# Optimization experiments

Measured on AMD Instinct MI355X. Metric: run time of the kernel, lower is better.

Reference implementation:

```python
import jax, jax.numpy as jnp
import numpy as np

B, T, E, H = 4, 2048, 1024, 16
HD = E // H  # head_size = 64


def setup_inputs() -> dict:
    key = jax.random.key(0)
    ks = jax.random.split(key, 6)
    s = 1.0 / np.sqrt(E)
    x = jax.random.normal(ks[0], (B, T, E), dtype=jnp.float32)
    # per-head Q/K/V projection weights, stacked over heads: [H, E, HD]
    Wq = jax.random.uniform(ks[1], (H, E, HD), minval=-s, maxval=s, dtype=jnp.float32)
    Wk = jax.random.uniform(ks[2], (H, E, HD), minval=-s, maxval=s, dtype=jnp.float32)
    Wv = jax.random.uniform(ks[3], (H, E, HD), minval=-s, maxval=s, dtype=jnp.float32)
    Wo = jax.random.uniform(ks[4], (E, E), minval=-s, maxval=s, dtype=jnp.float32)
    bo = jax.random.uniform(ks[5], (E,), minval=-s, maxval=s, dtype=jnp.float32)
    return {"x": x, "Wq": Wq, "Wk": Wk, "Wv": Wv, "Wo": Wo, "bo": bo}


def reference(x, Wq, Wk, Wv, Wo, bo):
    # x: [B,T,E] -> q,k,v: [B,H,T,HD]
    q = jnp.einsum('bte,hed->bhtd', x, Wq)
    k = jnp.einsum('bte,hed->bhtd', x, Wk)
    v = jnp.einsum('bte,hed->bhtd', x, Wv)
    scale = HD ** -0.5
    scores = jnp.einsum('bhtd,bhsd->bhts', q, k) * scale  # [B,H,T,T]
    causal = jnp.tril(jnp.ones((T, T), dtype=bool))
    scores = jnp.where(causal, scores, -jnp.inf)
    wei = jax.nn.softmax(scores, axis=-1)  # dropout is identity in eval
    out = jnp.einsum('bhts,bhsd->bhtd', wei, v)  # [B,H,T,HD]
    out = out.transpose(0, 2, 1, 3).reshape(B, T, E)  # concat heads
    return out @ Wo.T + bo
```

## Files before the change

kernel.cpp:

```cpp
#include <hip/hip_runtime.h>
#include <hip/hip_bf16.h>

#define B_  4
#define T_  2048
#define E_  1024
#define H_  16
#define HD_ 64

typedef __hip_bfloat16 bf16;
typedef unsigned short u16;
using bf16x8 = __attribute__((ext_vector_type(8))) short;
using f32x4  = __attribute__((ext_vector_type(4))) float;

__device__ __forceinline__ float b2f(bf16 x) { return __bfloat162float(x); }
__device__ __forceinline__ bf16  f2b(float x) { return __float2bfloat16(x); }
__device__ __forceinline__ u16 f2b_bits(float x) {
    union { bf16 h; u16 u; } cv; cv.h = __float2bfloat16(x); return cv.u;
}
__device__ __forceinline__ float bits2f(u16 u) {
    union { float f; unsigned int i; } cv; cv.i = ((unsigned int)u) << 16; return cv.f;
}

__device__ __forceinline__ void gld_lds16(const void* g, void* lds) {
    void* gv = (void*)g;
    __builtin_amdgcn_global_load_lds(
        (__attribute__((address_space(1))) void*)gv,
        (__attribute__((address_space(3))) void*)lds, 16, 0, 0);
}

__global__ __launch_bounds__(256) void cast_bf16(
    const float* __restrict__ src, bf16* __restrict__ dst)
{
    size_t i = ((size_t)blockIdx.x * 256 + threadIdx.x) * 8;
    float4 a = *(const float4*)(src + i);
    float4 b = *(const float4*)(src + i + 4);
    u16 o[8] = { f2b_bits(a.x), f2b_bits(a.y), f2b_bits(a.z), f2b_bits(a.w),
                 f2b_bits(b.x), f2b_bits(b.y), f2b_bits(b.z), f2b_bits(b.w) };
    *(uint4*)(dst + i) = *(const uint4*)o;
}

__global__ __launch_bounds__(256) void cast_w_t(
    const float* __restrict__ Wq, const float* __restrict__ Wk,
    const float* __restrict__ Wv, bf16* __restrict__ Wt)
{
    const float* W = (blockIdx.z == 0) ? Wq : (blockIdx.z == 1) ? Wk : Wv;
    const float scl = (blockIdx.z == 0) ? 0.125f : 1.0f;
    bf16* dst = Wt + (size_t)blockIdx.z * (H_ * HD_ * E_);
    const int h = blockIdx.y, k0 = blockIdx.x * 64;
    __shared__ float Ws[64][65];
    const int tid = threadIdx.x;
    {
        int kk = tid >> 2, d0 = (tid & 3) * 16;
        const float* p = W + ((size_t)h * E_ + k0 + kk) * HD_ + d0;
        #pragma unroll
        for (int i = 0; i < 4; i++) {
            float4 f = *(const float4*)(p + i * 4);
            Ws[kk][d0 + i * 4 + 0] = f.x; Ws[kk][d0 + i * 4 + 1] = f.y;
            Ws[kk][d0 + i * 4 + 2] = f.z; Ws[kk][d0 + i * 4 + 3] = f.w;
        }
    }
    __syncthreads();
    {
        int d = tid >> 2, kc = (tid & 3) * 16;
        u16 o[16];
        #pragma unroll
        for (int j = 0; j < 16; j++) o[j] = f2b_bits(Ws[kc + j][d] * scl);
        bf16* p = dst + ((size_t)h * HD_ + d) * E_ + k0 + kc;
        *(uint4*)(p)     = *(const uint4*)&o[0];
        *(uint4*)(p + 8) = *(const uint4*)&o[8];
    }
}

__global__ __launch_bounds__(256) void qkv_mfma(
    const bf16* __restrict__ xb, const bf16* __restrict__ Wt,
    bf16* __restrict__ q, bf16* __restrict__ k, bf16* __restrict__ v)
{
    const int n0 = blockIdx.x * 128;
    const int m0 = blockIdx.y * 128;
    const int z  = n0 >> 10;
    bf16* out = (z == 0) ? q : (z == 1) ? k : v;
    const int tid = threadIdx.x, lane = tid & 63, w = tid >> 6;
    const int wm = w >> 1, wn = w & 1;
    const int quad = lane >> 4, l15 = lane & 15;

    __shared__ __align__(16) u16 smem[2 * 128 * 64];
    u16* As = smem;
    u16* Bs = smem + 128 * 64;

    f32x4 acc[4][4];
    #pragma unroll
    for (int i = 0; i < 4; i++)
        #pragma unroll
        for (int j = 0; j < 4; j++) acc[i][j] = f32x4{0.f, 0.f, 0.f, 0.f};

    const int srow = lane >> 3;
    const int scol = ((lane & 7) ^ srow) * 8;
    const bf16* agp = xb + (size_t)(m0 + w * 32 + srow) * E_ + scol;
    const bf16* bgp = Wt + (size_t)(n0 + w * 32 + srow) * E_ + scol;
    u16* alds = As + (w * 32) * 64;
    u16* blds = Bs + (w * 32) * 64;
    const int rsw = l15 & 7;

    for (int k0 = 0; k0 < E_; k0 += 64) {
        __syncthreads();
        #pragma unroll
        for (int i = 0; i < 4; i++) {
            gld_lds16(agp + (size_t)(i * 8) * E_ + k0, alds + i * 8 * 64);
            gld_lds16(bgp + (size_t)(i * 8) * E_ + k0, blds + i * 8 * 64);
        }
        __syncthreads();

        #pragma unroll
        for (int ks = 0; ks < 2; ks++) {
            const int csw = ((ks * 4 + quad) ^ rsw) * 8;
            bf16x8 af[4];
            #pragma unroll
            for (int i = 0; i < 4; i++)
                af[i] = *(const bf16x8*)&As[(wm * 64 + i * 16 + l15) * 64 + csw];
            #pragma unroll
            for (int j = 0; j < 4; j++) {
                bf16x8 bfr = *(const bf16x8*)&Bs[(wn * 64 + j * 16 + l15) * 64 + csw];
                #pragma unroll
                for (int i = 0; i < 4; i++)
                    acc[i][j] = __builtin_amdgcn_mfma_f32_16x16x32_bf16(af[i], bfr, acc[i][j], 0, 0, 0);
            }
        }
    }

    if (z != 2) {
        const int h = ((n0 & 1023) >> 6) + wn;
        #pragma unroll
        for (int i = 0; i < 4; i++)
            #pragma unroll
            for (int r = 0; r < 4; r++) {
                int m = m0 + wm * 64 + i * 16 + quad * 4 + r;
                int bb2 = m >> 11, t = m & (T_ - 1);
                bf16* orow = out + ((size_t)(bb2 * H_ + h) * T_ + t) * HD_;
                #pragma unroll
                for (int j = 0; j < 4; j++)
                    orow[j * 16 + l15] = f2b(acc[i][j][r]);
            }
    } else {
        u16 (*Vt)[136] = (u16(*)[136])smem;
        const int bb2 = m0 >> 11, t0 = m0 & (T_ - 1);
        #pragma unroll
        for (int half = 0; half < 2; half++) {
            __syncthreads();
            if (wn == half) {
                #pragma unroll
                for (int j = 0; j < 4; j++)
                    #pragma unroll
                    for (int i = 0; i < 4; i++) {
                        ushort4 pk;
                        pk.x = f2b_bits(acc[i][j][0]);
                        pk.y = f2b_bits(acc[i][j][1]);
                        pk.z = f2b_bits(acc[i][j][2]);
                        pk.w = f2b_bits(acc[i][j][3]);
                        *(ushort4*)&Vt[j * 16 + l15][wm * 64 + i * 16 + quad * 4] = pk;
                    }
            }
            __syncthreads();
            {
                int dd = tid >> 2, tt = (tid & 3) * 32;
                int h = ((n0 & 1023) >> 6) + half;
                bf16* dst = out + ((size_t)(bb2 * H_ + h) * HD_ + dd) * T_ + t0 + tt;
                #pragma unroll
                for (int u = 0; u < 4; u++)
                    *(uint4*)(dst + u * 8) = *(const uint4*)&Vt[dd][tt + u * 8];
            }
        }
    }
}

__global__ __launch_bounds__(256) void flash_attn(
    const bf16* __restrict__ q, const bf16* __restrict__ k,
    const bf16* __restrict__ vt, bf16* __restrict__ att)
{
    const int bh = blockIdx.x & 63;
    const int qt = 31 - (blockIdx.x >> 6);
    const int q0 = qt * 64;
    const int hh = bh & 15, bb = bh >> 4;
    const int tid = threadIdx.x, lane = tid & 63, wave = tid >> 6;
    const int quad = lane >> 4, l15 = lane & 15;

    __shared__ __align__(16) u16 Ks[64 * 64];
    __shared__ __align__(16) u16 Vs[64 * 64];
    __shared__ __align__(16) u16 P2[4 * 1024];

    const size_t baseK = (size_t)bh * T_ * HD_;
    const bf16* vbase = vt + (size_t)bh * (size_t)HD_ * T_;

    const int qg = q0 + wave * 16 + l15;
    const bf16* qrow = q + baseK + (size_t)qg * HD_;
    bf16x8 qfrag[2];
    qfrag[0] = *(const bf16x8*)(qrow + quad * 8);
    qfrag[1] = *(const bf16x8*)(qrow + 32 + quad * 8);

    f32x4 o[4];
    #pragma unroll
    for (int dt = 0; dt < 4; dt++) o[dt] = f32x4{0.f, 0.f, 0.f, 0.f};
    float l_i = 0.f;

    const int q_in = wave * 16 + l15;

    const int srow = lane >> 3;
    const int scol = ((lane & 7) ^ srow) * 8;
    const bf16* kgp = k + baseK + (size_t)(wave * 16 + srow) * HD_ + scol;
    const bf16* vgp = vbase + (size_t)(wave * 16 + srow) * T_ + scol;
    u16* klds = Ks + wave * 16 * 64;
    u16* vlds = Vs + wave * 16 * 64;
    u16* pw = P2 + wave * 1024;
    const int rsw = l15 & 7;

    for (int st = 0; st <= qt; st++) {
        const int s0 = st * 64;
        __syncthreads();
        #pragma unroll
        for (int i = 0; i < 2; i++) {
            gld_lds16(kgp + (size_t)(s0 + i * 8) * HD_, klds + i * 8 * 64);
            gld_lds16(vgp + (size_t)(i * 8) * T_ + s0, vlds + i * 8 * 64);
        }
        __syncthreads();

        f32x4 s[4];
        #pragma unroll
        for (int ct = 0; ct < 4; ct++) {
            f32x4 a = f32x4{0.f, 0.f, 0.f, 0.f};
            #pragma unroll
            for (int ks = 0; ks < 2; ks++) {
                const int csw = ((ks * 4 + quad) ^ rsw) * 8;
                bf16x8 kfrag = *(const bf16x8*)&Ks[(ct * 16 + l15) * 64 + csw];
                a = __builtin_amdgcn_mfma_f32_16x16x32_bf16(kfrag, qfrag[ks], a, 0, 0, 0);
            }
            s[ct] = a;
        }

        if (st == qt) {
            #pragma unroll
            for (int ct = 0; ct < 4; ct++) {
                int sbase = ct * 16 + quad * 4;
                #pragma unroll
                for (int r = 0; r < 4; r++)
                    if (sbase + r > q_in) s[ct][r] = -1e30f;
            }
        }

        float rsum = 0.f;
        #pragma unroll
        for (int ct = 0; ct < 4; ct++) {
            ushort4 pk;
            pk.x = f2b_bits(__expf(s[ct][0] - 8.0f));
            pk.y = f2b_bits(__expf(s[ct][1] - 8.0f));
            pk.z = f2b_bits(__expf(s[ct][2] - 8.0f));
            pk.w = f2b_bits(__expf(s[ct][3] - 8.0f));
            rsum += bits2f(pk.x) + bits2f(pk.y) + bits2f(pk.z) + bits2f(pk.w);
            *(ushort4*)&pw[(ct >> 1) * 512
                           + (((((ct & 1) << 1) | (quad >> 1)) * 16 + l15) * 8)
                           + (quad & 1) * 4] = pk;
        }
        rsum += __shfl_xor(rsum, 16, 64);
        rsum += __shfl_xor(rsum, 32, 64);
        l_i += rsum;

        #pragma unroll
        for (int ks = 0; ks < 2; ks++) {
            bf16x8 pfrag = *(const bf16x8*)&pw[ks * 512 + (quad * 16 + l15) * 8];
            #pragma unroll
            for (int dt = 0; dt < 4; dt++) {
                const int csw = ((ks * 4 + quad) ^ rsw) * 8;
                bf16x8 vfrag = *(const bf16x8*)&Vs[(dt * 16 + l15) * 64 + csw];
                o[dt] = __builtin_amdgcn_mfma_f32_16x16x32_bf16(vfrag, pfrag, o[dt], 0, 0, 0);
            }
        }
    }

    float inv = 1.0f / l_i;
    bf16* orow = att + ((size_t)(bb * T_ + qg) * H_ + hh) * HD_;
    #pragma unroll
    for (int dt = 0; dt < 4; dt++) {
        ushort4 pk;
        pk.x = f2b_bits(o[dt][0] * inv);
        pk.y = f2b_bits(o[dt][1] * inv);
        pk.z = f2b_bits(o[dt][2] * inv);
        pk.w = f2b_bits(o[dt][3] * inv);
        *(ushort4*)(orow + dt * 16 + quad * 4) = pk;
    }
}

__global__ __launch_bounds__(256, 3) void out_proj_mfma(
    const bf16* __restrict__ att, const bf16* __restrict__ Wob,
    const float* __restrict__ bo, float* __restrict__ out)
{
    const int m0 = blockIdx.x * 128, n0 = blockIdx.y * 128;
    const int tid = threadIdx.x, lane = tid & 63, w = tid >> 6;
    const int wm = w >> 1, wn = w & 1;
    const int quad = lane >> 4, l15 = lane & 15;

    __shared__ __align__(16) u16 As[128 * 32];
    __shared__ __align__(16) u16 Bs[128 * 32];

    f32x4 acc[4][4];
    #pragma unroll
    for (int i = 0; i < 4; i++)
        #pragma unroll
        for (int j = 0; j < 4; j++) acc[i][j] = f32x4{0.f, 0.f, 0.f, 0.f};

    const int srow = lane >> 2;
    const int scol = ((lane & 3) ^ (srow & 3)) * 8;
    const bf16* agp = att + (size_t)(m0 + w * 32 + srow) * E_ + scol;
    const bf16* bgp = Wob + (size_t)(n0 + w * 32 + srow) * E_ + scol;
    u16* alds = As + (w * 32) * 32;
    u16* blds = Bs + (w * 32) * 32;
    const int rsw3 = l15 & 3;

    for (int k0 = 0; k0 < E_; k0 += 32) {
        __syncthreads();
        #pragma unroll
        for (int i = 0; i < 2; i++) {
            gld_lds16(agp + (size_t)(i * 16) * E_ + k0, alds + i * 16 * 32);
            gld_lds16(bgp + (size_t)(i * 16) * E_ + k0, blds + i * 16 * 32);
        }
        __syncthreads();

        const int csw = (quad ^ rsw3) * 8;
        bf16x8 af[4];
        #pragma unroll
        for (int i = 0; i < 4; i++)
            af[i] = *(const bf16x8*)&As[(wm * 64 + i * 16 + l15) * 32 + csw];
        #pragma unroll
        for (int j = 0; j < 4; j++) {
            bf16x8 bfr = *(const bf16x8*)&Bs[(wn * 64 + j * 16 + l15) * 32 + csw];
            #pragma unroll
            for (int i = 0; i < 4; i++)
                acc[i][j] = __builtin_amdgcn_mfma_f32_16x16x32_bf16(af[i], bfr, acc[i][j], 0, 0, 0);
        }
    }

    float bias[4];
    #pragma unroll
    for (int j = 0; j < 4; j++) bias[j] = bo[n0 + wn * 64 + j * 16 + l15];
    #pragma unroll
    for (int i = 0; i < 4; i++)
        #pragma unroll
        for (int r = 0; r < 4; r++) {
            int m = m0 + wm * 64 + i * 16 + quad * 4 + r;
            float* orow = out + (size_t)m * E_ + n0 + wn * 64;
            #pragma unroll
            for (int j = 0; j < 4; j++)
                orow[j * 16 + l15] = acc[i][j][r] + bias[j];
        }
}

extern "C" void kernel_launch(void* const* d_in, const int* in_sizes, int n_in,
                              void* d_out, int out_size, void* d_ws, size_t ws_size,
                              hipStream_t stream)
{
    const float* x  = (const float*)d_in[0];
    const float* Wq = (const float*)d_in[1];
    const float* Wk = (const float*)d_in[2];
    const float* Wv = (const float*)d_in[3];
    const float* Wo = (const float*)d_in[4];
    const float* bo = (const float*)d_in[5];
    float* out = (float*)d_out;

    const size_t elts = (size_t)B_ * H_ * T_ * HD_;
    bf16* att = (bf16*)d_ws;
    bf16* Wt  = att;
    bf16* q   = att + elts;
    bf16* Wob = q;
    bf16* k   = q + elts;
    bf16* v   = k + elts;
    bf16* xb  = (bf16*)d_out;

    cast_bf16<<<dim3((unsigned)(elts / 2048)), 256, 0, stream>>>(x, xb);
    cast_w_t<<<dim3(E_ / 64, H_, 3), 256, 0, stream>>>(Wq, Wk, Wv, Wt);

    qkv_mfma<<<dim3(3 * E_ / 128, (B_ * T_) / 128), 256, 0, stream>>>(xb, Wt, q, k, v);

    flash_attn<<<dim3((T_ / 64) * B_ * H_), 256, 0, stream>>>(q, k, v, att);

    cast_bf16<<<dim3((E_ * E_) / 2048), 256, 0, stream>>>(Wo, Wob);

    out_proj_mfma<<<dim3((B_ * T_) / 128, E_ / 128), 256, 0, stream>>>(att, Wob, bo, out);
}
```

Before: 253.2 us.

## Double-buffer K/V tiles in flash attention and compute row sums via MFMA

Adds double-buffered LDS for the K and V tiles so that the global-to-LDS load of the next tile is issued before computing on the current one, using an explicit vmcnt wait and raw barriers in place of two __syncthreads per step. The softmax row sum is now produced by an extra MFMA against a vector of ones instead of per-lane adds and cross-lane shuffles. The exponential is rewritten as exp2 of a fused multiply-add, and setprio hints are placed around the MFMA sections. LDS use grows to hold the second buffer, which could lower occupancy, and correctness relies on the hand-written waitcnt count matching the number of issued loads.

```diff
diff --git a/kernel.cpp b/kernel.cpp
--- a/kernel.cpp
+++ b/kernel.cpp
@@ -183,9 +183,9 @@
     const int tid = threadIdx.x, lane = tid & 63, wave = tid >> 6;
     const int quad = lane >> 4, l15 = lane & 15;
 
-    __shared__ __align__(16) u16 Ks[64 * 64];
-    __shared__ __align__(16) u16 Vs[64 * 64];
-    __shared__ __align__(16) u16 P2[4 * 1024];
+    __shared__ __align__(16) u16 Ks[2][64 * 64];
+    __shared__ __align__(16) u16 Vs[2][64 * 64];
+    __shared__ __align__(16) u16 P2[4][1024];
 
     const size_t baseK = (size_t)bh * T_ * HD_;
     const bf16* vbase = vt + (size_t)bh * (size_t)HD_ * T_;
@@ -196,10 +196,14 @@
     qfrag[0] = *(const bf16x8*)(qrow + quad * 8);
     qfrag[1] = *(const bf16x8*)(qrow + 32 + quad * 8);
 
+    bf16x8 onesf;
+    #pragma unroll
+    for (int i = 0; i < 8; i++) onesf[i] = (short)0x3F80;
+
     f32x4 o[4];
     #pragma unroll
     for (int dt = 0; dt < 4; dt++) o[dt] = f32x4{0.f, 0.f, 0.f, 0.f};
-    float l_i = 0.f;
+    f32x4 lacc = f32x4{0.f, 0.f, 0.f, 0.f};
 
     const int q_in = wave * 16 + l15;
 
@@ -207,33 +211,43 @@
     const int scol = ((lane & 7) ^ srow) * 8;
     const bf16* kgp = k + baseK + (size_t)(wave * 16 + srow) * HD_ + scol;
     const bf16* vgp = vbase + (size_t)(wave * 16 + srow) * T_ + scol;
-    u16* klds = Ks + wave * 16 * 64;
-    u16* vlds = Vs + wave * 16 * 64;
-    u16* pw = P2 + wave * 1024;
+    u16* pw = P2[wave];
     const int rsw = l15 & 7;
 
+    #define STAGE(b, s0) do {                                                 \
+        gld_lds16(kgp + (size_t)(s0) * HD_,       &Ks[b][wave * 1024]);       \
+        gld_lds16(kgp + (size_t)((s0) + 8) * HD_, &Ks[b][wave * 1024 + 512]); \
+        gld_lds16(vgp + (s0),                     &Vs[b][wave * 1024]);       \
+        gld_lds16(vgp + (s0) + 8 * T_,            &Vs[b][wave * 1024 + 512]); \
+    } while (0)
+
+    STAGE(0, 0);
+    int cur = 0;
+
     for (int st = 0; st <= qt; st++) {
-        const int s0 = st * 64;
-        __syncthreads();
-        #pragma unroll
-        for (int i = 0; i < 2; i++) {
-            gld_lds16(kgp + (size_t)(s0 + i * 8) * HD_, klds + i * 8 * 64);
-            gld_lds16(vgp + (size_t)(i * 8) * T_ + s0, vlds + i * 8 * 64);
-        }
-        __syncthreads();
+        if (st < qt) {
+            STAGE(cur ^ 1, (st + 1) * 64);
+            asm volatile("s_waitcnt vmcnt(4)" ::: "memory");
+        } else {
+            asm volatile("s_waitcnt vmcnt(0)" ::: "memory");
+        }
+        __builtin_amdgcn_s_barrier();
+        __builtin_amdgcn_sched_barrier(0);
 
         f32x4 s[4];
+        __builtin_amdgcn_s_setprio(1);
         #pragma unroll
         for (int ct = 0; ct < 4; ct++) {
             f32x4 a = f32x4{0.f, 0.f, 0.f, 0.f};
             #pragma unroll
             for (int ks = 0; ks < 2; ks++) {
                 const int csw = ((ks * 4 + quad) ^ rsw) * 8;
-                bf16x8 kfrag = *(const bf16x8*)&Ks[(ct * 16 + l15) * 64 + csw];
+                bf16x8 kfrag = *(const bf16x8*)&Ks[cur][(ct * 16 + l15) * 64 + csw];
                 a = __builtin_amdgcn_mfma_f32_16x16x32_bf16(kfrag, qfrag[ks], a, 0, 0, 0);
             }
             s[ct] = a;
         }
+        __builtin_amdgcn_s_setprio(0);
 
         if (st == qt) {
             #pragma unroll
@@ -245,36 +259,39 @@
             }
         }
 
-        float rsum = 0.f;
         #pragma unroll
         for (int ct = 0; ct < 4; ct++) {
             ushort4 pk;
-            pk.x = f2b_bits(__expf(s[ct][0] - 8.0f));
-            pk.y = f2b_bits(__expf(s[ct][1] - 8.0f));
-            pk.z = f2b_bits(__expf(s[ct][2] - 8.0f));
-            pk.w = f2b_bits(__expf(s[ct][3] - 8.0f));
-            rsum += bits2f(pk.x) + bits2f(pk.y) + bits2f(pk.z) + bits2f(pk.w);
+            pk.x = f2b_bits(__builtin_amdgcn_exp2f(__fmaf_rn(s[ct][0], 1.4426950408889634f, -11.541560327111707f)));
+            pk.y = f2b_bits(__builtin_amdgcn_exp2f(__fmaf_rn(s[ct][1], 1.4426950408889634f, -11.541560327111707f)));
+            pk.z = f2b_bits(__builtin_amdgcn_exp2f(__fmaf_rn(s[ct][2], 1.4426950408889634f, -11.541560327111707f)));
+            pk.w = f2b_bits(__builtin_amdgcn_exp2f(__fmaf_rn(s[ct][3], 1.4426950408889634f, -11.541560327111707f)));
             *(ushort4*)&pw[(ct >> 1) * 512
                            + (((((ct & 1) << 1) | (quad >> 1)) * 16 + l15) * 8)
                            + (quad & 1) * 4] = pk;
         }
-        rsum += __shfl_xor(rsum, 16, 64);
-        rsum += __shfl_xor(rsum, 32, 64);
-        l_i += rsum;
-
+
+        __builtin_amdgcn_s_setprio(1);
         #pragma unroll
         for (int ks = 0; ks < 2; ks++) {
             bf16x8 pfrag = *(const bf16x8*)&pw[ks * 512 + (quad * 16 + l15) * 8];
+            lacc = __builtin_amdgcn_mfma_f32_16x16x32_bf16(onesf, pfrag, lacc, 0, 0, 0);
             #pragma unroll
             for (int dt = 0; dt < 4; dt++) {
                 const int csw = ((ks * 4 + quad) ^ rsw) * 8;
-                bf16x8 vfrag = *(const bf16x8*)&Vs[(dt * 16 + l15) * 64 + csw];
+                bf16x8 vfrag = *(const bf16x8*)&Vs[cur][(dt * 16 + l15) * 64 + csw];
                 o[dt] = __builtin_amdgcn_mfma_f32_16x16x32_bf16(vfrag, pfrag, o[dt], 0, 0, 0);
             }
         }
-    }
-
-    float inv = 1.0f / l_i;
+        __builtin_amdgcn_s_setprio(0);
+
+        __builtin_amdgcn_sched_barrier(0);
+        __builtin_amdgcn_s_barrier();
+        cur ^= 1;
+    }
+    #undef STAGE
+
+    float inv = 1.0f / lacc[0];
     bf16* orow = att + ((size_t)(bb * T_ + qg) * H_ + hh) * HD_;
     #pragma unroll
     for (int dt = 0; dt < 4; dt++) {
```

New measurement: 245.7 us. 3.0% less time.
